# Optimization experiments

Measured on AMD Instinct MI355X. Metric: run time of the kernel, lower is better.

Reference implementation:

```python
import jax, jax.numpy as jnp
import numpy as np

N_NODES = 50000
N_EDGES = 800000
IN_CH, HID_CH, OUT_CH = 128, 256, 128


def setup_inputs() -> dict:
    key = jax.random.key(0)
    ks = jax.random.split(key, 9)
    x = jax.random.normal(ks[0], (N_NODES, IN_CH), dtype=jnp.float32)
    edge_index = jax.random.randint(ks[1], (2, N_EDGES), 0, N_NODES, dtype=jnp.int64)
    # SAGEConv params: lin_l (aggregated neighbors, with bias), lin_r (root, no bias)
    s1 = 1.0 / np.sqrt(IN_CH)
    s2 = 1.0 / np.sqrt(HID_CH)
    W1_l = jax.random.uniform(ks[2], (IN_CH, HID_CH), jnp.float32, -s1, s1)
    W1_r = jax.random.uniform(ks[3], (IN_CH, HID_CH), jnp.float32, -s1, s1)
    b1 = jax.random.uniform(ks[4], (HID_CH,), jnp.float32, -s1, s1)
    W2_l = jax.random.uniform(ks[5], (HID_CH, OUT_CH), jnp.float32, -s2, s2)
    W2_r = jax.random.uniform(ks[6], (HID_CH, OUT_CH), jnp.float32, -s2, s2)
    b2 = jax.random.uniform(ks[7], (OUT_CH,), jnp.float32, -s2, s2)
    return {"x": x, "edge_index": edge_index, "W1_l": W1_l, "W1_r": W1_r,
            "b1": b1, "W2_l": W2_l, "W2_r": W2_r, "b2": b2}


def _sage_conv(x, edge_index, Wl, Wr, b):
    # PyG SAGEConv: out = lin_l(mean_{j in N(i)} x_j) + lin_r(x_i)
    src, dst = edge_index[0], edge_index[1]
    msg = x[src]                                                    # [E, C] gather
    agg = jax.ops.segment_sum(msg, dst, num_segments=x.shape[0])    # [N, C] scatter-add
    cnt = jax.ops.segment_sum(jnp.ones((src.shape[0],), x.dtype), dst,
                              num_segments=x.shape[0])              # [N]
    agg = agg / jnp.maximum(cnt, 1.0)[:, None]                      # mean; deg-0 -> 0
    return agg @ Wl + x @ Wr + b


def reference(x, edge_index, W1_l, W1_r, b1, W2_l, W2_r, b2):
    h = jax.nn.relu(_sage_conv(x, edge_index, W1_l, W1_r, b1))
    # dropout(p=0.5) is stochastic; use eval-mode identity for a deterministic baseline
    out = _sage_conv(h, edge_index, W2_l, W2_r, b2)
    return jax.nn.log_softmax(out, axis=1)
```

## Files before the change

### kernel.cpp

```cpp
#include <hip/hip_runtime.h>
#include <math.h>

#define NN 50000
#define NE 800000
#define BINW 256
#define NB ((NN + BINW - 1) / BINW)
#define CAP 4864
#define CHUNK 4096
#define NBIN ((NE + CHUNK - 1) / CHUNK)
#define NXB 6250
#define NWB 256
#define EPT 16

typedef __attribute__((ext_vector_type(8))) short short8;
typedef __attribute__((ext_vector_type(4))) float f32x4;
typedef unsigned int uint32;
typedef __attribute__((address_space(3))) unsigned int lds_uint;
typedef const __attribute__((address_space(1))) unsigned int glb_uint;

__device__ inline unsigned short f2bf(float f) {
    unsigned u = __builtin_bit_cast(unsigned, f);
    u += 0x7FFF + ((u >> 16) & 1);
    return (unsigned short)(u >> 16);
}
__device__ inline float bf_lo(uint32 v) { return __builtin_bit_cast(float, v << 16); }
__device__ inline float bf_hi(uint32 v) { return __builtin_bit_cast(float, v & 0xFFFF0000u); }

__device__ inline int edge_at(const void* edges, int is64, int i) {
    return is64 ? (int)((const long long*)edges)[i] : ((const int*)edges)[i];
}

__global__ void k_zero(int* bcnt) {
    int i = threadIdx.x;
    if (i < NB) bcnt[i] = 0;
}

__global__ __launch_bounds__(256)
void k_front(const void* __restrict__ edges, uint32* __restrict__ gbuf,
             int* __restrict__ bcnt,
             const float* __restrict__ x, unsigned short* __restrict__ A1,
             const float* __restrict__ W1l, const float* __restrict__ W1r,
             const float* __restrict__ W2l, const float* __restrict__ W2r,
             unsigned short* __restrict__ B1t, unsigned short* __restrict__ B2t) {
    int b = blockIdx.x;
    if (b >= NBIN) {
        if (b < NBIN + NXB) {
            int t = (b - NBIN) * 256 + threadIdx.x;
            if (t >= NN * 32) return;
            int node = t >> 5, q = t & 31;
            float4 v = *(const float4*)(x + (size_t)node * 128 + q * 4);
            uint32 p0 = f2bf(v.x) | ((uint32)f2bf(v.y) << 16);
            uint32 p1 = f2bf(v.z) | ((uint32)f2bf(v.w) << 16);
            *(uint2*)(A1 + (size_t)node * 256 + 128 + q * 4) = make_uint2(p0, p1);
        } else {
            int t = (b - NBIN - NXB) * 256 + threadIdx.x;
            int n = t >> 8, k = t & 255;
            float v1 = (k < 128) ? W1l[k * 256 + n] : W1r[(k - 128) * 256 + n];
            B1t[n * 256 + k] = f2bf(v1);
            float v2 = (n < 128) ? W2l[k * 128 + n] : W2r[k * 128 + (n - 128)];
            B2t[n * 256 + k] = f2bf(v2);
        }
        return;
    }
    __shared__ int hist[NB], excl[NB], cur[NB], gpos[NB];
    __shared__ int is64s;
    __shared__ uint32 sorted[CHUNK];
    int t = threadIdx.x;
    int base = b * CHUNK;
    int n = NE - base; if (n > CHUNK) n = CHUNK;
    if (t < 64) {
        const long long* q = (const long long*)edges;
        long long v = q[t];
        unsigned long long m = __ballot(v >= 0 && v < NN);
        if (t == 0) is64s = (m == ~0ull) ? 1 : 0;
    }
    for (int i = t; i < NB; i += 256) hist[i] = 0;
    __syncthreads();
    int is64 = is64s;
    int sA[EPT], dA[EPT];
    #pragma unroll
    for (int q = 0; q < EPT; ++q) {
        int i = t + q * 256;
        if (i < n) {
            sA[q] = edge_at(edges, is64, base + i);
            dA[q] = edge_at(edges, is64, NE + base + i);
        } else dA[q] = -1;
    }
    #pragma unroll
    for (int q = 0; q < EPT; ++q)
        if (dA[q] >= 0) atomicAdd(&hist[dA[q] >> 8], 1);
    __syncthreads();
    if (t == 0) {
        int s = 0;
        for (int k = 0; k < NB; ++k) { excl[k] = s; s += hist[k]; }
    }
    __syncthreads();
    for (int i = t; i < NB; i += 256) {
        gpos[i] = atomicAdd(&bcnt[i], hist[i]);
        cur[i] = excl[i];
    }
    __syncthreads();
    #pragma unroll
    for (int q = 0; q < EPT; ++q) {
        if (dA[q] >= 0) {
            int bk = dA[q] >> 8;
            int lp = atomicAdd(&cur[bk], 1);
            sorted[lp] = ((uint32)(dA[q] & (BINW - 1)) << 16) | (uint32)sA[q];
        }
    }
    __syncthreads();
    for (int i = t; i < n; i += 256) {
        int lo = 0, hi = NB - 1;
        while (lo < hi) { int mid = (lo + hi + 1) >> 1; if (excl[mid] <= i) lo = mid; else hi = mid - 1; }
        int gp = gpos[lo] + (i - excl[lo]);
        if (gp < CAP) gbuf[(size_t)lo * CAP + gp] = sorted[i];
    }
}

__global__ void k_bbase(const int* __restrict__ bcnt, int* __restrict__ bbase,
                        int* __restrict__ offs) {
    __shared__ int wsum[4], tot;
    int t = threadIdx.x, lane = t & 63, w = t >> 6;
    int d = (t < NB) ? bcnt[t] : 0;
    int v = d;
    #pragma unroll
    for (int s = 1; s < 64; s <<= 1) { int x = __shfl_up(v, s); if (lane >= s) v += x; }
    if (lane == 63) wsum[w] = v;
    __syncthreads();
    if (t == 0) {
        int s = 0;
        for (int i = 0; i < 4; ++i) { int x = wsum[i]; wsum[i] = s; s += x; }
        tot = s;
    }
    __syncthreads();
    int excl = wsum[w] + (v - d);
    if (t < NB) bbase[t] = excl;
    if (t == 0) offs[NN] = tot;
}

__global__ __launch_bounds__(256) void k_sort(const uint32* __restrict__ gbuf,
                                              const int* __restrict__ bcnt,
                                              const int* __restrict__ bbase,
                                              int* __restrict__ offs,
                                              unsigned short* __restrict__ ssrc) {
    __shared__ int hist[BINW], cur[BINW], wsum[4];
    __shared__ int sorted[CAP];
    int b = blockIdx.x, t = threadIdx.x;
    int cnt = bcnt[b]; if (cnt > CAP) cnt = CAP;
    int bb = bbase[b];
    int nbase = b * BINW;
    int ncnt = NN - nbase; if (ncnt > BINW) ncnt = BINW;
    if (t < BINW) hist[t] = 0;
    __syncthreads();
    for (int i = t; i < cnt; i += 256)
        atomicAdd(&hist[gbuf[(size_t)b * CAP + i] >> 16], 1);
    __syncthreads();
    int lane = t & 63, w = t >> 6;
    int d = hist[t];
    int v = d;
    #pragma unroll
    for (int s = 1; s < 64; s <<= 1) { int x = __shfl_up(v, s); if (lane >= s) v += x; }
    if (lane == 63) wsum[w] = v;
    __syncthreads();
    if (t == 0) { int s = 0; for (int i = 0; i < 4; ++i) { int x = wsum[i]; wsum[i] = s; s += x; } }
    __syncthreads();
    int excl = wsum[w] + (v - d);
    if (t < ncnt) offs[nbase + t] = bb + excl;
    cur[t] = excl;
    __syncthreads();
    for (int i = t; i < cnt; i += 256) {
        uint32 p = gbuf[(size_t)b * CAP + i];
        int lp = atomicAdd(&cur[p >> 16], 1);
        sorted[lp] = (int)(p & 0xFFFFu);
    }
    __syncthreads();
    for (int i = t; i < cnt; i += 256)
        ssrc[bb + i] = (unsigned short)sorted[i];
}

#define ACC8(vv) { a[0] += bf_lo((vv).x); a[1] += bf_hi((vv).x); \
                   a[2] += bf_lo((vv).y); a[3] += bf_hi((vv).y); \
                   a[4] += bf_lo((vv).z); a[5] += bf_hi((vv).z); \
                   a[6] += bf_lo((vv).w); a[7] += bf_hi((vv).w); }

__device__ inline void burst_gather4(const unsigned short* __restrict__ tab, int coff,
                                     const unsigned short* __restrict__ ssrc, int s0, int s1,
                                     int lane, float* a) {
    int grp = lane >> 4, cl = lane & 15;
    const unsigned short* bp = tab + coff + cl * 8;
    int e = s0;
    while (e < s1) {
        int cnt = s1 - e; if (cnt > 64) cnt = 64;
        int myidx = (lane < cnt) ? (int)ssrc[e + lane] : 0;
        for (int r0 = 0; r0 < cnt; r0 += 32) {
            uint4 v[8]; bool ok[8];
            #pragma unroll
            for (int u = 0; u < 8; ++u) {
                int r = r0 + u * 4 + grp;
                ok[u] = r < cnt;
                int s = __shfl(myidx, r & 63);
                v[u] = *(const uint4*)(bp + (size_t)s * 256);
            }
            #pragma unroll
            for (int u = 0; u < 8; ++u) if (ok[u]) ACC8(v[u]);
        }
        e += cnt;
    }
}

__device__ inline void xreduce8(float* a) {
    #pragma unroll
    for (int k = 0; k < 8; ++k) {
        a[k] += __shfl_xor(a[k], 16);
        a[k] += __shfl_xor(a[k], 32);
    }
}

__global__ void k_agg(unsigned short* __restrict__ A1, const int* __restrict__ offs,
                      const unsigned short* __restrict__ ssrc) {
    int node = blockIdx.x * 4 + (threadIdx.x >> 6);
    int lane = threadIdx.x & 63;
    if (node >= NN) return;
    int cl = lane & 15;
    int s0 = offs[node], s1 = offs[node + 1];
    float a[8] = {};
    burst_gather4(A1, 128, ssrc, s0, s1, lane, a);
    xreduce8(a);
    float inv = 1.0f / fmaxf((float)(s1 - s0), 1.0f);
    if (lane < 16) {
        uint4 p;
        p.x = f2bf(a[0] * inv) | ((uint32)f2bf(a[1] * inv) << 16);
        p.y = f2bf(a[2] * inv) | ((uint32)f2bf(a[3] * inv) << 16);
        p.z = f2bf(a[4] * inv) | ((uint32)f2bf(a[5] * inv) << 16);
        p.w = f2bf(a[6] * inv) | ((uint32)f2bf(a[7] * inv) << 16);
        *(uint4*)(A1 + (size_t)node * 256 + cl * 8) = p;
    }
}

template <bool RELU>
__global__ __launch_bounds__(256)
void k_gemm_bf(const unsigned short* __restrict__ A, const unsigned short* __restrict__ Bt,
               const float* __restrict__ bias, unsigned short* __restrict__ C) {
    __shared__ unsigned short AsmL[2][128 * 32];
    __shared__ unsigned short BsmL[2][128 * 32];
    int t = threadIdx.x;
    int lane = t & 63, w = t >> 6;
    int m0 = blockIdx.x * 128, n0 = blockIdx.y * 128;
    int wr = (w >> 1) * 64, wc = (w & 1) * 64;
    int fr = lane & 15, fk = (lane >> 4) * 8;

    f32x4 acc[4][4] = {};
    int srow = lane >> 2;
    int scol = (lane & 3) * 8;
    auto STAGE = [&](int bufi, int ks) {
        #pragma unroll
        for (int q = 0; q < 2; ++q) {
            int widx = w * 2 + q;
            int row = widx * 16 + srow;
            const unsigned short* ga = A + (size_t)(m0 + row) * 256 + ks * 32 + scol;
            __builtin_amdgcn_global_load_lds((glb_uint*)ga, (lds_uint*)&AsmL[bufi][widx * 512], 16, 0, 0);
            const unsigned short* gb = Bt + (size_t)(n0 + row) * 256 + ks * 32 + scol;
            __builtin_amdgcn_global_load_lds((glb_uint*)gb, (lds_uint*)&BsmL[bufi][widx * 512], 16, 0, 0);
        }
    };

    STAGE(0, 0);
    __syncthreads();
    int cur = 0;
    #pragma unroll
    for (int ks = 0; ks < 8; ++ks) {
        if (ks < 7) STAGE(cur ^ 1, ks + 1);
        short8 af[4], bfr[4];
        #pragma unroll
        for (int i = 0; i < 4; ++i) af[i] = *(const short8*)&AsmL[cur][(wr + i * 16 + fr) * 32 + fk];
        #pragma unroll
        for (int j = 0; j < 4; ++j) bfr[j] = *(const short8*)&BsmL[cur][(wc + j * 16 + fr) * 32 + fk];
        #pragma unroll
        for (int i = 0; i < 4; ++i)
            #pragma unroll
            for (int j = 0; j < 4; ++j)
                acc[i][j] = __builtin_amdgcn_mfma_f32_16x16x32_bf16(af[i], bfr[j], acc[i][j], 0, 0, 0);
        if (ks < 7) {
            __syncthreads();
            cur ^= 1;
        }
    }

    int r0 = (lane >> 4) * 4;
    #pragma unroll
    for (int i = 0; i < 4; ++i) {
        #pragma unroll
        for (int j = 0; j < 4; ++j) {
            int gn = n0 + wc + j * 16 + fr;
            float bb = RELU ? bias[gn] : 0.f;
            #pragma unroll
            for (int rr = 0; rr < 4; ++rr) {
                int gm = m0 + wr + i * 16 + r0 + rr;
                if (gm >= NN) continue;
                float v = acc[i][j][rr];
                if (RELU) v = fmaxf(v + bb, 0.f);
                C[(size_t)gm * 256 + gn] = f2bf(v);
            }
        }
    }
}

__global__ void k_final(const unsigned short* __restrict__ P, const int* __restrict__ offs,
                        const unsigned short* __restrict__ ssrc, const float* __restrict__ b2,
                        float* __restrict__ out) {
    int node = blockIdx.x * 4 + (threadIdx.x >> 6);
    int lane = threadIdx.x & 63;
    if (node >= NN) return;
    int cl = lane & 15;
    int s0 = offs[node], s1 = offs[node + 1];
    float a[8] = {};
    burst_gather4(P, 0, ssrc, s0, s1, lane, a);
    xreduce8(a);
    float inv = 1.0f / fmaxf((float)(s1 - s0), 1.0f);
    uint4 rv = *(const uint4*)(P + (size_t)node * 256 + 128 + cl * 8);
    float4 ba = *(const float4*)(b2 + cl * 8);
    float4 bb = *(const float4*)(b2 + cl * 8 + 4);
    float vv[8];
    vv[0] = a[0] * inv + bf_lo(rv.x) + ba.x;
    vv[1] = a[1] * inv + bf_hi(rv.x) + ba.y;
    vv[2] = a[2] * inv + bf_lo(rv.y) + ba.z;
    vv[3] = a[3] * inv + bf_hi(rv.y) + ba.w;
    vv[4] = a[4] * inv + bf_lo(rv.z) + bb.x;
    vv[5] = a[5] * inv + bf_hi(rv.z) + bb.y;
    vv[6] = a[6] * inv + bf_lo(rv.w) + bb.z;
    vv[7] = a[7] * inv + bf_hi(rv.w) + bb.w;

    float mx = vv[0];
    #pragma unroll
    for (int k = 1; k < 8; ++k) mx = fmaxf(mx, vv[k]);
    #pragma unroll
    for (int d = 1; d < 16; d <<= 1) mx = fmaxf(mx, __shfl_xor(mx, d));
    float s = 0.f;
    #pragma unroll
    for (int k = 0; k < 8; ++k) s += __expf(vv[k] - mx);
    #pragma unroll
    for (int d = 1; d < 16; d <<= 1) s += __shfl_xor(s, d);
    float ls = logf(s);
    if (lane < 16) {
        float4 o0 = make_float4(vv[0] - mx - ls, vv[1] - mx - ls, vv[2] - mx - ls, vv[3] - mx - ls);
        float4 o1 = make_float4(vv[4] - mx - ls, vv[5] - mx - ls, vv[6] - mx - ls, vv[7] - mx - ls);
        *(float4*)(out + (size_t)node * 128 + cl * 8) = o0;
        *(float4*)(out + (size_t)node * 128 + cl * 8 + 4) = o1;
    }
}

extern "C" void kernel_launch(void* const* d_in, const int* in_sizes, int n_in,
                              void* d_out, int out_size, void* d_ws, size_t ws_size,
                              hipStream_t stream) {
    const float* x   = (const float*)d_in[0];
    const void*  edg = d_in[1];
    const float* W1l = (const float*)d_in[2];
    const float* W1r = (const float*)d_in[3];
    const float* b1  = (const float*)d_in[4];
    const float* W2l = (const float*)d_in[5];
    const float* W2r = (const float*)d_in[6];
    const float* b2  = (const float*)d_in[7];
    float* out = (float*)d_out;

    char* ws = (char*)d_ws;
    size_t off = 0;
    auto alloc = [&](size_t bytes) {
        size_t cur = off;
        off = (off + bytes + 255) & ~(size_t)255;
        return cur;
    };
    int* bcnt  = (int*)(ws + alloc((size_t)NB * 4));
    int* bbase = (int*)(ws + alloc((size_t)NB * 4));
    int* offs  = (int*)(ws + alloc((size_t)(NN + 1) * 4));
    unsigned short* ssrc = (unsigned short*)(ws + alloc((size_t)NE * 2));
    uint32* gbuf = (uint32*)(ws + alloc((size_t)NB * CAP * 4));
    unsigned short* A1  = (unsigned short*)(ws + alloc((size_t)NN * 256 * 2));
    unsigned short* Hb  = (unsigned short*)(ws + alloc((size_t)NN * 256 * 2));
    unsigned short* Pb  = (unsigned short*)(ws + alloc((size_t)NN * 256 * 2));
    unsigned short* B1t = (unsigned short*)(ws + alloc((size_t)65536 * 2));
    unsigned short* B2t = (unsigned short*)(ws + alloc((size_t)65536 * 2));
    (void)alloc(65536);

    int nb_w = (NN + 3) / 4;
    int mblocks = (NN + 127) / 128;

    k_zero<<<1, 256, 0, stream>>>(bcnt);
    k_front<<<NBIN + NXB + NWB, 256, 0, stream>>>(edg, gbuf, bcnt, x, A1,
                                                  W1l, W1r, W2l, W2r, B1t, B2t);
    k_bbase<<<1, 256, 0, stream>>>(bcnt, bbase, offs);
    k_sort<<<NB, 256, 0, stream>>>(gbuf, bcnt, bbase, offs, ssrc);
    k_agg<<<nb_w, 256, 0, stream>>>(A1, offs, ssrc);
    k_gemm_bf<true><<<dim3(mblocks, 2), 256, 0, stream>>>(A1, B1t, b1, Hb);
    k_gemm_bf<false><<<dim3(mblocks, 2), 256, 0, stream>>>(Hb, B2t, nullptr, Pb);
    k_final<<<nb_w, 256, 0, stream>>>(Pb, offs, ssrc, b2, out);
}
```

Baseline: 150.6 us.

## Fold bucket prefix into sort kernel and triple-buffer GEMM LDS staging

Removes the single-block k_bbase launch. Each k_sort block now computes its own base offset by reducing the bucket counts of all earlier buckets, and the last block writes offs[NN]=NE. The GEMM moves from double to triple buffering of LDS tiles, using explicit vmcnt waits and raw barriers so two stages of global-to-LDS loads stay in flight. This cuts one launch and a serial dependency and aims to hide load latency, at the cost of more LDS per block and fragile hand-written wait counts. Setting offs[NN] to NE assumes no bucket overflowed CAP.

```diff
diff --git a/kernel.cpp b/kernel.cpp
--- a/kernel.cpp
+++ b/kernel.cpp
@@ -117,45 +117,31 @@
     }
 }
 
-__global__ void k_bbase(const int* __restrict__ bcnt, int* __restrict__ bbase,
-                        int* __restrict__ offs) {
-    __shared__ int wsum[4], tot;
-    int t = threadIdx.x, lane = t & 63, w = t >> 6;
-    int d = (t < NB) ? bcnt[t] : 0;
-    int v = d;
-    #pragma unroll
-    for (int s = 1; s < 64; s <<= 1) { int x = __shfl_up(v, s); if (lane >= s) v += x; }
-    if (lane == 63) wsum[w] = v;
-    __syncthreads();
-    if (t == 0) {
-        int s = 0;
-        for (int i = 0; i < 4; ++i) { int x = wsum[i]; wsum[i] = s; s += x; }
-        tot = s;
-    }
-    __syncthreads();
-    int excl = wsum[w] + (v - d);
-    if (t < NB) bbase[t] = excl;
-    if (t == 0) offs[NN] = tot;
-}
-
 __global__ __launch_bounds__(256) void k_sort(const uint32* __restrict__ gbuf,
                                               const int* __restrict__ bcnt,
-                                              const int* __restrict__ bbase,
                                               int* __restrict__ offs,
                                               unsigned short* __restrict__ ssrc) {
     __shared__ int hist[BINW], cur[BINW], wsum[4];
     __shared__ int sorted[CAP];
+    __shared__ int bb_s;
     int b = blockIdx.x, t = threadIdx.x;
+    int lane = t & 63, w = t >> 6;
+    int c = (t < NB) ? bcnt[t] : 0;
+    int pre = (t < b) ? c : 0;
+    #pragma unroll
+    for (int s = 1; s < 64; s <<= 1) pre += __shfl_xor(pre, s);
+    if (lane == 0) wsum[w] = pre;
+    hist[t] = 0;
+    __syncthreads();
+    if (t == 0) bb_s = wsum[0] + wsum[1] + wsum[2] + wsum[3];
+    __syncthreads();
+    int bb = bb_s;
     int cnt = bcnt[b]; if (cnt > CAP) cnt = CAP;
-    int bb = bbase[b];
     int nbase = b * BINW;
     int ncnt = NN - nbase; if (ncnt > BINW) ncnt = BINW;
-    if (t < BINW) hist[t] = 0;
-    __syncthreads();
     for (int i = t; i < cnt; i += 256)
         atomicAdd(&hist[gbuf[(size_t)b * CAP + i] >> 16], 1);
     __syncthreads();
-    int lane = t & 63, w = t >> 6;
     int d = hist[t];
     int v = d;
     #pragma unroll
@@ -166,6 +152,7 @@
     __syncthreads();
     int excl = wsum[w] + (v - d);
     if (t < ncnt) offs[nbase + t] = bb + excl;
+    if (b == NB - 1 && t == 0) offs[NN] = NE;
     cur[t] = excl;
     __syncthreads();
     for (int i = t; i < cnt; i += 256) {
@@ -241,8 +228,8 @@
 __global__ __launch_bounds__(256)
 void k_gemm_bf(const unsigned short* __restrict__ A, const unsigned short* __restrict__ Bt,
                const float* __restrict__ bias, unsigned short* __restrict__ C) {
-    __shared__ unsigned short AsmL[2][128 * 32];
-    __shared__ unsigned short BsmL[2][128 * 32];
+    __shared__ unsigned short AsmL[3][128 * 32];
+    __shared__ unsigned short BsmL[3][128 * 32];
     int t = threadIdx.x;
     int lane = t & 63, w = t >> 6;
     int m0 = blockIdx.x * 128, n0 = blockIdx.y * 128;
@@ -265,25 +252,25 @@
     };
 
     STAGE(0, 0);
-    __syncthreads();
-    int cur = 0;
+    STAGE(1, 1);
     #pragma unroll
     for (int ks = 0; ks < 8; ++ks) {
-        if (ks < 7) STAGE(cur ^ 1, ks + 1);
+        if (ks < 7) asm volatile("s_waitcnt vmcnt(4)" ::: "memory");
+        else        asm volatile("s_waitcnt vmcnt(0)" ::: "memory");
+        __builtin_amdgcn_s_barrier();
+        __builtin_amdgcn_sched_barrier(0);
+        if (ks < 6) STAGE((ks + 2) % 3, ks + 2);
+        int cb = ks % 3;
         short8 af[4], bfr[4];
         #pragma unroll
-        for (int i = 0; i < 4; ++i) af[i] = *(const short8*)&AsmL[cur][(wr + i * 16 + fr) * 32 + fk];
-        #pragma unroll
-        for (int j = 0; j < 4; ++j) bfr[j] = *(const short8*)&BsmL[cur][(wc + j * 16 + fr) * 32 + fk];
+        for (int i = 0; i < 4; ++i) af[i] = *(const short8*)&AsmL[cb][(wr + i * 16 + fr) * 32 + fk];
+        #pragma unroll
+        for (int j = 0; j < 4; ++j) bfr[j] = *(const short8*)&BsmL[cb][(wc + j * 16 + fr) * 32 + fk];
         #pragma unroll
         for (int i = 0; i < 4; ++i)
             #pragma unroll
             for (int j = 0; j < 4; ++j)
                 acc[i][j] = __builtin_amdgcn_mfma_f32_16x16x32_bf16(af[i], bfr[j], acc[i][j], 0, 0, 0);
-        if (ks < 7) {
-            __syncthreads();
-            cur ^= 1;
-        }
     }
 
     int r0 = (lane >> 4) * 4;
@@ -370,7 +357,6 @@
         return cur;
     };
     int* bcnt  = (int*)(ws + alloc((size_t)NB * 4));
-    int* bbase = (int*)(ws + alloc((size_t)NB * 4));
     int* offs  = (int*)(ws + alloc((size_t)(NN + 1) * 4));
     unsigned short* ssrc = (unsigned short*)(ws + alloc((size_t)NE * 2));
     uint32* gbuf = (uint32*)(ws + alloc((size_t)NB * CAP * 4));
@@ -387,8 +373,7 @@
     k_zero<<<1, 256, 0, stream>>>(bcnt);
     k_front<<<NBIN + NXB + NWB, 256, 0, stream>>>(edg, gbuf, bcnt, x, A1,
                                                   W1l, W1r, W2l, W2r, B1t, B2t);
-    k_bbase<<<1, 256, 0, stream>>>(bcnt, bbase, offs);
-    k_sort<<<NB, 256, 0, stream>>>(gbuf, bcnt, bbase, offs, ssrc);
+    k_sort<<<NB, 256, 0, stream>>>(gbuf, bcnt, offs, ssrc);
     k_agg<<<nb_w, 256, 0, stream>>>(A1, offs, ssrc);
     k_gemm_bf<true><<<dim3(mblocks, 2), 256, 0, stream>>>(A1, B1t, b1, Hb);
     k_gemm_bf<false><<<dim3(mblocks, 2), 256, 0, stream>>>(Hb, B2t, nullptr, Pb);
```

Measured after the change: 149.5 us. Within noise of the previous version (-0.8%).
